# Kernel optimization log

Hardware: AMD Instinct MI355X
Metric: run time of the kernel (lower is better)

Reference implementation:

```python
import jax, jax.numpy as jnp
import numpy as np

D_MODEL = 1024
N_HEADS = 16
D_K = D_MODEL // N_HEADS  # 64
B, T = 2, 2048


def setup_inputs() -> dict:
    key = jax.random.key(0)
    ks = jax.random.split(key, 6)
    s = 0.02
    x = jax.random.normal(ks[0], (B, T, D_MODEL), dtype=jnp.float32)
    # Stacked per-head projection weights, [H, C, d_k] (no bias, mini-gpt style)
    Wq = jax.random.normal(ks[1], (N_HEADS, D_MODEL, D_K), dtype=jnp.float32) * s
    Wk = jax.random.normal(ks[2], (N_HEADS, D_MODEL, D_K), dtype=jnp.float32) * s
    Wv = jax.random.normal(ks[3], (N_HEADS, D_MODEL, D_K), dtype=jnp.float32) * s
    # Output projection, torch nn.Linear(d_model, d_model): y = x @ Wo.T + bo
    Wo = jax.random.normal(ks[4], (D_MODEL, D_MODEL), dtype=jnp.float32) * s
    bo = jax.random.normal(ks[5], (D_MODEL,), dtype=jnp.float32) * s
    return {"x": x, "Wq": Wq, "Wk": Wk, "Wv": Wv, "Wo": Wo, "bo": bo}


def reference(x, Wq, Wk, Wv, Wo, bo):
    Bq, Tq, C = x.shape
    # Batched per-head projections (replaces the per-head Python loop)
    q = jnp.einsum('btc,hck->bhtk', x, Wq)  # [B,H,T,dk]
    k = jnp.einsum('btc,hck->bhtk', x, Wk)
    v = jnp.einsum('btc,hck->bhtk', x, Wv)
    scale = 1.0 / jnp.sqrt(jnp.asarray(D_K, dtype=x.dtype))
    scores = jnp.einsum('bhtk,bhsk->bhts', q, k) * scale  # [B,H,T,T]
    causal = jnp.tril(jnp.ones((Tq, Tq), dtype=bool))
    scores = jnp.where(causal, scores, jnp.asarray(-1e9, dtype=scores.dtype))
    attn = jax.nn.softmax(scores, axis=-1)
    out = jnp.einsum('bhts,bhsk->bhtk', attn, v)  # [B,H,T,dk]
    # concat heads -> [B,T,C]
    out = out.transpose(0, 2, 1, 3).reshape(Bq, Tq, C)
    return jnp.einsum('btc,dc->btd', out, Wo) + bo
```

## Files before the change

kernel.cpp:

```cpp
#include <hip/hip_runtime.h>
#include <hip/hip_bf16.h>


using short8 = __attribute__((ext_vector_type(8))) short;
using f32x4  = __attribute__((ext_vector_type(4))) float;
using fp16x2 = __attribute__((ext_vector_type(2))) __fp16;
using half4  = __attribute__((ext_vector_type(4))) _Float16;
using half8  = __attribute__((ext_vector_type(8))) _Float16;

#define SCALE_LOG2E 0.18033688011112042f

__device__ __forceinline__ unsigned short f2bf(float f) {
    union { float f; unsigned u; } v; v.f = f;
    unsigned r = v.u + 0x7fffu + ((v.u >> 16) & 1u);
    return (unsigned short)(r >> 16);
}

__device__ __forceinline__ void gld16(const unsigned short* gp, unsigned short* lp) {
    __builtin_amdgcn_global_load_lds(
        (const __attribute__((address_space(1))) void*)(gp),
        (__attribute__((address_space(3))) void*)(unsigned int)(unsigned long long)(lp),
        16, 0, 0);
}

__global__ void cvt_bf16(const float* __restrict__ in,
                         unsigned short* __restrict__ out, int n4) {
    int i = blockIdx.x * blockDim.x + threadIdx.x;
    if (i >= n4) return;
    float4 v = ((const float4*)in)[i];
    ushort4 o;
    o.x = f2bf(v.x); o.y = f2bf(v.y); o.z = f2bf(v.z); o.w = f2bf(v.w);
    ((ushort4*)out)[i] = o;
}

__global__ void transpose_w(const float* __restrict__ Wq,
                            const float* __restrict__ Wk,
                            const float* __restrict__ Wv,
                            unsigned short* __restrict__ wfrag) {
    __shared__ float tile[64][65];
    int b = blockIdx.x;
    int cchunk = b & 15;
    int h = (b >> 4) & 15;
    int s = b >> 8;
    const float* W = (s == 0) ? Wq : ((s == 1) ? Wk : Wv);
    float sc = (s == 0) ? SCALE_LOG2E : 1.0f;
    const float* src = W + (h * 1024 + cchunk * 64) * 64;
    int t = threadIdx.x;
    #pragma unroll
    for (int it = 0; it < 4; ++it) {
        int idx = (it * 256 + t) * 4;
        int cc = idx >> 6, kk = idx & 63;
        float4 v = *(const float4*)(src + idx);
        tile[cc][kk + 0] = v.x; tile[cc][kk + 1] = v.y;
        tile[cc][kk + 2] = v.z; tile[cc][kk + 3] = v.w;
    }
    __syncthreads();
    int sh = s * 16 + h;
    #pragma unroll
    for (int p = 0; p < 2; ++p) {
        int slot = p * 256 + t;
        int d   = slot & 63;
        int cc8 = slot >> 6;
        int n16  = sh * 4 + (d >> 4);
        int col  = d & 15;
        int kq   = cchunk * 2 + (cc8 >> 2);
        int quad = cc8 & 3;
        ushort4 lo, hi;
        lo.x = f2bf(tile[cc8 * 8 + 0][d] * sc); lo.y = f2bf(tile[cc8 * 8 + 1][d] * sc);
        lo.z = f2bf(tile[cc8 * 8 + 2][d] * sc); lo.w = f2bf(tile[cc8 * 8 + 3][d] * sc);
        hi.x = f2bf(tile[cc8 * 8 + 4][d] * sc); hi.y = f2bf(tile[cc8 * 8 + 5][d] * sc);
        hi.z = f2bf(tile[cc8 * 8 + 6][d] * sc); hi.w = f2bf(tile[cc8 * 8 + 7][d] * sc);
        unsigned short* dst = wfrag + ((size_t)((n16 * 32 + kq) * 64 + quad * 16 + col)) * 8;
        *(ushort4*)dst = lo;
        *(ushort4*)(dst + 4) = hi;
    }
}

__global__ void wo_frag(const float* __restrict__ Wo,
                        unsigned short* __restrict__ wofrag) {
    int g = blockIdx.x * 256 + threadIdx.x;
    int col  = g & 15;
    int quad = (g >> 4) & 3;
    int kq   = (g >> 6) & 31;
    int n16  = g >> 11;
    const float* src = Wo + (size_t)(n16 * 16 + col) * 1024 + kq * 32 + quad * 8;
    float4 a = *(const float4*)src;
    float4 b = *(const float4*)(src + 4);
    ushort4 lo, hi;
    lo.x = f2bf(a.x); lo.y = f2bf(a.y); lo.z = f2bf(a.z); lo.w = f2bf(a.w);
    hi.x = f2bf(b.x); hi.y = f2bf(b.y); hi.z = f2bf(b.z); hi.w = f2bf(b.w);
    *(ushort4*)(wofrag + (size_t)g * 8)     = lo;
    *(ushort4*)(wofrag + (size_t)g * 8 + 4) = hi;
}

__global__ __launch_bounds__(128, 4) void qkv_gemm(
        const unsigned short* __restrict__ xb,
        const unsigned short* __restrict__ wtf,
        unsigned short* __restrict__ qB,
        unsigned short* __restrict__ kfrag,
        _Float16* __restrict__ vfrag) {
    __shared__ unsigned short Als[64 * 32];
    int wave = threadIdx.x >> 6;
    int lane = threadIdx.x & 63;
    int col  = lane & 15;
    int quad = lane >> 4;
    int ldr = lane >> 2;
    int ldc = ((lane & 3) ^ ((lane >> 3) & 3)) * 8;
    int swq = (quad ^ ((col >> 1) & 3)) * 8;
    int m0 = blockIdx.x * 64;
    int n0 = blockIdx.y * 128 + wave * 64;
    int n16b = n0 >> 4;
    f32x4 acc[4][4] = {};
    for (int k0 = 0; k0 < 1024; k0 += 32) {
        int kq = k0 >> 5;
        __syncthreads();
        short8 bf[4];
        #pragma unroll
        for (int nb = 0; nb < 4; ++nb)
            bf[nb] = *(const short8*)(wtf +
                ((size_t)((n16b + nb) * 32 + kq) * 64 + lane) * 8);
        #pragma unroll
        for (int j = 0; j < 2; ++j) {
            int row = wave * 32 + j * 16;
            gld16(xb + (size_t)(m0 + row + ldr) * 1024 + k0 + ldc, Als + row * 32);
        }
        __syncthreads();
        short8 af[4];
        #pragma unroll
        for (int i = 0; i < 4; ++i)
            af[i] = *(const short8*)(Als + (i * 16 + col) * 32 + swq);
        #pragma unroll
        for (int mb = 0; mb < 4; ++mb)
            #pragma unroll
            for (int nb = 0; nb < 4; ++nb)
                acc[mb][nb] = __builtin_amdgcn_mfma_f32_16x16x32_bf16(
                    af[mb], bf[nb], acc[mb][nb], 0, 0, 0);
    }
    int sel = blockIdx.y >> 3;
    #pragma unroll
    for (int nb = 0; nb < 4; ++nb) {
        int n = n0 + nb * 16 + col;
        int d10 = n & 1023;
        int h_ = d10 >> 6, d = d10 & 63;
        if (sel == 0) {
            #pragma unroll
            for (int mb = 0; mb < 4; ++mb)
                #pragma unroll
                for (int r = 0; r < 4; ++r) {
                    int m = m0 + mb * 16 + quad * 4 + r;
                    int b_ = m >> 11, t_ = m & 2047;
                    qB[((size_t)(b_ * 16 + h_) * 2048 + t_) * 64 + d] =
                        f2bf(acc[mb][nb][r]);
                }
        } else if (sel == 1) {
            int hK = d >> 5, quadk = (d >> 3) & 3, j = d & 7;
            #pragma unroll
            for (int mb = 0; mb < 4; ++mb)
                #pragma unroll
                for (int r = 0; r < 4; ++r) {
                    int m = m0 + mb * 16 + quad * 4 + r;
                    int b_ = m >> 11, t_ = m & 2047;
                    int bh = b_ * 16 + h_;
                    kfrag[((((size_t)bh * 128 + (t_ >> 4)) * 2 + hK) * 64 +
                           quadk * 16 + (t_ & 15)) * 8 + j] = f2bf(acc[mb][nb][r]);
                }
        } else {
            int nbv = d >> 4, colv = d & 15;
            #pragma unroll
            for (int mb = 0; mb < 4; ++mb) {
                int m = m0 + mb * 16 + quad * 4;
                int b_ = m >> 11, t_ = m & 2047;
                int bh = b_ * 16 + h_;
                half4 hv;
                hv[0] = (_Float16)acc[mb][nb][0]; hv[1] = (_Float16)acc[mb][nb][1];
                hv[2] = (_Float16)acc[mb][nb][2]; hv[3] = (_Float16)acc[mb][nb][3];
                *(half4*)(vfrag + ((((size_t)bh * 64 + (t_ >> 5)) * 4 + nbv) * 64 +
                          ((t_ >> 2) & 3) * 16 + colv) * 8 + ((t_ >> 4) & 1) * 4) = hv;
            }
        }
    }
}

__global__ __launch_bounds__(128, 4) void oproj(
        const unsigned short* __restrict__ A,
        const unsigned short* __restrict__ wof,
        const float* __restrict__ bo,
        float* __restrict__ y) {
    __shared__ unsigned short Als[32 * 32];
    int wave = threadIdx.x >> 6;
    int lane = threadIdx.x & 63;
    int col  = lane & 15;
    int quad = lane >> 4;
    int ldr = lane >> 2;
    int ldc = ((lane & 3) ^ ((lane >> 3) & 3)) * 8;
    int swq = (quad ^ ((col >> 1) & 3)) * 8;
    int m0 = blockIdx.x * 32;
    int n0 = blockIdx.y * 128 + wave * 64;
    int n16b = n0 >> 4;
    f32x4 acc[2][4] = {};
    for (int k0 = 0; k0 < 1024; k0 += 32) {
        int kq = k0 >> 5;
        __syncthreads();
        short8 bf[4];
        #pragma unroll
        for (int nb = 0; nb < 4; ++nb)
            bf[nb] = *(const short8*)(wof +
                ((size_t)((n16b + nb) * 32 + kq) * 64 + lane) * 8);
        gld16(A + (size_t)(m0 + wave * 16 + ldr) * 1024 + k0 + ldc,
              Als + (wave * 16) * 32);
        __syncthreads();
        short8 af[2];
        #pragma unroll
        for (int i = 0; i < 2; ++i)
            af[i] = *(const short8*)(Als + (i * 16 + col) * 32 + swq);
        #pragma unroll
        for (int mb = 0; mb < 2; ++mb)
            #pragma unroll
            for (int nb = 0; nb < 4; ++nb)
                acc[mb][nb] = __builtin_amdgcn_mfma_f32_16x16x32_bf16(
                    af[mb], bf[nb], acc[mb][nb], 0, 0, 0);
    }
    #pragma unroll
    for (int nb = 0; nb < 4; ++nb) {
        int n = n0 + nb * 16 + col;
        float bias = bo[n];
        #pragma unroll
        for (int mb = 0; mb < 2; ++mb)
            #pragma unroll
            for (int r = 0; r < 4; ++r) {
                int m = m0 + mb * 16 + quad * 4 + r;
                y[(size_t)m * 1024 + n] = acc[mb][nb][r] + bias;
            }
    }
}

__global__ __launch_bounds__(256, 3) void attn(
        const unsigned short* __restrict__ qB,
        const unsigned short* __restrict__ kfrag,
        const _Float16* __restrict__ vfrag,
        unsigned short* __restrict__ aout) {
    __shared__ float O_comb[2][64][33];
    __shared__ float L_comb[2][2][2][16];
    int wave = threadIdx.x >> 6;
    int lane = threadIdx.x & 63;
    int col  = lane & 15;
    int quad = lane >> 4;
    int sl     = wave >> 1;
    int parity = wave & 1;
    int bh   = blockIdx.x & 31;
    int pairidx = 31 - (blockIdx.x >> 5);
    int strip = pairidx * 2 + sl;
    int q0 = strip * 32;
    const unsigned short* q = qB + (size_t)bh * 2048 * 64;
    const unsigned short* kf_base = kfrag + (size_t)bh * 128 * 2 * 512;
    const _Float16*       vf_base = vfrag + (size_t)bh * 64 * 4 * 512;

    short8 qf[2][2];
    #pragma unroll
    for (int qb = 0; qb < 2; ++qb)
        #pragma unroll
        for (int h = 0; h < 2; ++h)
            qf[qb][h] = *(const short8*)(q + (size_t)(q0 + qb * 16 + col) * 64 + h * 32 + quad * 8);

    f32x4 o[2][4] = {};
    float l[2] = {0.f, 0.f};

    struct KV { short8 kf[2][2]; half8 vv[4]; };
    KV bufA, bufB;

    auto load_half = [&](int it, int kv32, KV& b) {
        int K16 = it * 4 + kv32 * 2;
        #pragma unroll
        for (int p = 0; p < 2; ++p)
            #pragma unroll
            for (int h = 0; h < 2; ++h)
                b.kf[p][h] = *(const short8*)(kf_base +
                    (((size_t)(K16 + p) * 2 + h) * 64 + lane) * 8);
        #pragma unroll
        for (int nb = 0; nb < 4; ++nb)
            b.vv[nb] = *(const half8*)(vf_base +
                (((size_t)(it * 2 + kv32) * 4 + nb) * 64 + lane) * 8);
    };

    auto compute_half = [&](int it, int kv32, KV& b) {
        int kv0 = it * 64;
        bool diag = (kv0 + 63 > q0);
        #pragma unroll
        for (int par = 0; par < 2; ++par) {
            int kvbase = kv0 + kv32 * 32 + par * 16;
            f32x4 st[2] = {};
            #pragma unroll
            for (int qb = 0; qb < 2; ++qb) {
                st[qb] = __builtin_amdgcn_mfma_f32_16x16x32_bf16(b.kf[par][0], qf[qb][0], st[qb], 0, 0, 0);
                st[qb] = __builtin_amdgcn_mfma_f32_16x16x32_bf16(b.kf[par][1], qf[qb][1], st[qb], 0, 0, 0);
            }
            #pragma unroll
            for (int qb = 0; qb < 2; ++qb) {
                float p0 = __builtin_amdgcn_exp2f(st[qb][0]);
                float p1 = __builtin_amdgcn_exp2f(st[qb][1]);
                float p2 = __builtin_amdgcn_exp2f(st[qb][2]);
                float p3 = __builtin_amdgcn_exp2f(st[qb][3]);
                if (diag) {
                    int qg  = q0 + qb * 16 + col;
                    int kvg = kvbase + quad * 4;
                    p0 = (kvg + 0 > qg) ? 0.f : p0;
                    p1 = (kvg + 1 > qg) ? 0.f : p1;
                    p2 = (kvg + 2 > qg) ? 0.f : p2;
                    p3 = (kvg + 3 > qg) ? 0.f : p3;
                }
                l[qb] += (p0 + p1) + (p2 + p3);
                union { fp16x2 h2[2]; half4 h4; } cvt;
                cvt.h2[0] = __builtin_amdgcn_cvt_pkrtz(p0, p1);
                cvt.h2[1] = __builtin_amdgcn_cvt_pkrtz(p2, p3);
                half4 pf = cvt.h4;
                #pragma unroll
                for (int nb = 0; nb < 4; ++nb) {
                    half4 vf = (par == 0)
                        ? __builtin_shufflevector(b.vv[nb], b.vv[nb], 0, 1, 2, 3)
                        : __builtin_shufflevector(b.vv[nb], b.vv[nb], 4, 5, 6, 7);
                    o[qb][nb] = __builtin_amdgcn_mfma_f32_16x16x16f16(pf, vf, o[qb][nb], 0, 0, 0);
                }
            }
        }
    };

    int n_iter = (q0 + 95) >> 6;
    if (parity < n_iter) load_half(parity, 0, bufA);
    for (int it = parity; it < n_iter; it += 2) {
        load_half(it, 1, bufB);
        compute_half(it, 0, bufA);
        if (it + 2 < n_iter) load_half(it + 2, 0, bufA);
        compute_half(it, 1, bufB);
    }

    #pragma unroll
    for (int qb = 0; qb < 2; ++qb) {
        float lr = l[qb];
        lr += __shfl_xor(lr, 16);
        lr += __shfl_xor(lr, 32);
        l[qb] = lr;
    }
    if (quad == 0) {
        L_comb[sl][parity][0][col] = l[0];
        L_comb[sl][parity][1][col] = l[1];
    }
    if (parity == 1) {
        #pragma unroll
        for (int qb = 0; qb < 2; ++qb)
            #pragma unroll
            for (int nb = 0; nb < 4; ++nb)
                #pragma unroll
                for (int r = 0; r < 4; ++r)
                    O_comb[sl][lane][qb * 16 + nb * 4 + r] = o[qb][nb][r];
    }
    __syncthreads();
    if (parity == 0) {
        int b_ = bh >> 4, h_ = bh & 15;
        #pragma unroll
        for (int qb = 0; qb < 2; ++qb)
            #pragma unroll
            for (int r = 0; r < 4; ++r) {
                int qi = quad * 4 + r;
                float inv_l = 1.0f / (L_comb[sl][0][qb][qi] + L_comb[sl][1][qb][qi]);
                int t_ = q0 + qb * 16 + qi;
                #pragma unroll
                for (int nb = 0; nb < 4; ++nb) {
                    float ov = o[qb][nb][r] + O_comb[sl][lane][qb * 16 + nb * 4 + r];
                    aout[(size_t)(b_ * 2048 + t_) * 1024 + h_ * 64 + nb * 16 + col] =
                        f2bf(ov * inv_l);
                }
            }
    }
}

extern "C" void kernel_launch(void* const* d_in, const int* in_sizes, int n_in,
                              void* d_out, int out_size, void* d_ws, size_t ws_size,
                              hipStream_t stream) {
    const float* x  = (const float*)d_in[0];
    const float* Wq = (const float*)d_in[1];
    const float* Wk = (const float*)d_in[2];
    const float* Wv = (const float*)d_in[3];
    const float* Wo = (const float*)d_in[4];
    const float* bo = (const float*)d_in[5];
    float* y = (float*)d_out;

    unsigned short* xb    = (unsigned short*)d_ws;
    unsigned short* Wtf   = xb    + 4194304;
    unsigned short* Wof   = Wtf   + 3145728;
    unsigned short* qBb   = Wof   + 1048576;
    unsigned short* kfr   = qBb   + 4194304;
    unsigned short* vfr   = kfr   + 4194304;
    unsigned short* aout  = vfr   + 4194304;

    cvt_bf16<<<4096, 256, 0, stream>>>(x, xb, 1048576);
    transpose_w<<<768, 256, 0, stream>>>(Wq, Wk, Wv, Wtf);
    wo_frag<<<512, 256, 0, stream>>>(Wo, Wof);
    qkv_gemm<<<dim3(64, 24), 128, 0, stream>>>(xb, Wtf, qBb, kfr, (_Float16*)vfr);
    attn<<<1024, 256, 0, stream>>>(qBb, kfr, (const _Float16*)vfr, aout);
    oproj<<<dim3(128, 8), 128, 0, stream>>>(aout, Wof, bo, y);
}
```

Measured before the change: 169.5 us.

## Merge prep kernels and double-buffer QKV and output projection GEMMs

Folds the three preprocessing kernels (x cast, QKV weight fragment transpose, Wo fragment build) into one launch that dispatches on block index, which cuts launch overhead. Both projection GEMMs switch to double-buffered LDS staging with register-prefetched B fragments, so the loads for the next K step overlap the MFMA work on the current one. The QKV GEMM also moves to 256-thread blocks covering 128 rows, so each B fragment feeds more rows, at the cost of twice the LDS and fewer blocks.

```diff
diff --git a/kernel.cpp b/kernel.cpp
--- a/kernel.cpp
+++ b/kernel.cpp
@@ -23,83 +23,85 @@
         16, 0, 0);
 }
 
-__global__ void cvt_bf16(const float* __restrict__ in,
-                         unsigned short* __restrict__ out, int n4) {
-    int i = blockIdx.x * blockDim.x + threadIdx.x;
-    if (i >= n4) return;
-    float4 v = ((const float4*)in)[i];
-    ushort4 o;
-    o.x = f2bf(v.x); o.y = f2bf(v.y); o.z = f2bf(v.z); o.w = f2bf(v.w);
-    ((ushort4*)out)[i] = o;
-}
-
-__global__ void transpose_w(const float* __restrict__ Wq,
-                            const float* __restrict__ Wk,
-                            const float* __restrict__ Wv,
-                            unsigned short* __restrict__ wfrag) {
+__global__ void prep(const float* __restrict__ x,
+                     const float* __restrict__ Wq,
+                     const float* __restrict__ Wk,
+                     const float* __restrict__ Wv,
+                     const float* __restrict__ Wo,
+                     unsigned short* __restrict__ xb,
+                     unsigned short* __restrict__ wfrag,
+                     unsigned short* __restrict__ wofrag) {
     __shared__ float tile[64][65];
-    int b = blockIdx.x;
-    int cchunk = b & 15;
-    int h = (b >> 4) & 15;
-    int s = b >> 8;
-    const float* W = (s == 0) ? Wq : ((s == 1) ? Wk : Wv);
-    float sc = (s == 0) ? SCALE_LOG2E : 1.0f;
-    const float* src = W + (h * 1024 + cchunk * 64) * 64;
+    int blk = blockIdx.x;
     int t = threadIdx.x;
-    #pragma unroll
-    for (int it = 0; it < 4; ++it) {
-        int idx = (it * 256 + t) * 4;
-        int cc = idx >> 6, kk = idx & 63;
-        float4 v = *(const float4*)(src + idx);
-        tile[cc][kk + 0] = v.x; tile[cc][kk + 1] = v.y;
-        tile[cc][kk + 2] = v.z; tile[cc][kk + 3] = v.w;
-    }
-    __syncthreads();
-    int sh = s * 16 + h;
-    #pragma unroll
-    for (int p = 0; p < 2; ++p) {
-        int slot = p * 256 + t;
-        int d   = slot & 63;
-        int cc8 = slot >> 6;
-        int n16  = sh * 4 + (d >> 4);
-        int col  = d & 15;
-        int kq   = cchunk * 2 + (cc8 >> 2);
-        int quad = cc8 & 3;
+    if (blk < 768) {
+        int b = blk;
+        int cchunk = b & 15;
+        int h = (b >> 4) & 15;
+        int s = b >> 8;
+        const float* W = (s == 0) ? Wq : ((s == 1) ? Wk : Wv);
+        float sc = (s == 0) ? SCALE_LOG2E : 1.0f;
+        const float* src = W + (h * 1024 + cchunk * 64) * 64;
+        #pragma unroll
+        for (int it = 0; it < 4; ++it) {
+            int idx = (it * 256 + t) * 4;
+            int cc = idx >> 6, kk = idx & 63;
+            float4 v = *(const float4*)(src + idx);
+            tile[cc][kk + 0] = v.x; tile[cc][kk + 1] = v.y;
+            tile[cc][kk + 2] = v.z; tile[cc][kk + 3] = v.w;
+        }
+        __syncthreads();
+        int sh = s * 16 + h;
+        #pragma unroll
+        for (int p = 0; p < 2; ++p) {
+            int slot = p * 256 + t;
+            int d   = slot & 63;
+            int cc8 = slot >> 6;
+            int n16  = sh * 4 + (d >> 4);
+            int col  = d & 15;
+            int kq   = cchunk * 2 + (cc8 >> 2);
+            int quad = cc8 & 3;
+            ushort4 lo, hi;
+            lo.x = f2bf(tile[cc8 * 8 + 0][d] * sc); lo.y = f2bf(tile[cc8 * 8 + 1][d] * sc);
+            lo.z = f2bf(tile[cc8 * 8 + 2][d] * sc); lo.w = f2bf(tile[cc8 * 8 + 3][d] * sc);
+            hi.x = f2bf(tile[cc8 * 8 + 4][d] * sc); hi.y = f2bf(tile[cc8 * 8 + 5][d] * sc);
+            hi.z = f2bf(tile[cc8 * 8 + 6][d] * sc); hi.w = f2bf(tile[cc8 * 8 + 7][d] * sc);
+            unsigned short* dst = wfrag + ((size_t)((n16 * 32 + kq) * 64 + quad * 16 + col)) * 8;
+            *(ushort4*)dst = lo;
+            *(ushort4*)(dst + 4) = hi;
+        }
+    } else if (blk < 1280) {
+        int g = (blk - 768) * 256 + t;
+        int col  = g & 15;
+        int quad = (g >> 4) & 3;
+        int kq   = (g >> 6) & 31;
+        int n16  = g >> 11;
+        const float* src = Wo + (size_t)(n16 * 16 + col) * 1024 + kq * 32 + quad * 8;
+        float4 a = *(const float4*)src;
+        float4 b2 = *(const float4*)(src + 4);
         ushort4 lo, hi;
-        lo.x = f2bf(tile[cc8 * 8 + 0][d] * sc); lo.y = f2bf(tile[cc8 * 8 + 1][d] * sc);
-        lo.z = f2bf(tile[cc8 * 8 + 2][d] * sc); lo.w = f2bf(tile[cc8 * 8 + 3][d] * sc);
-        hi.x = f2bf(tile[cc8 * 8 + 4][d] * sc); hi.y = f2bf(tile[cc8 * 8 + 5][d] * sc);
-        hi.z = f2bf(tile[cc8 * 8 + 6][d] * sc); hi.w = f2bf(tile[cc8 * 8 + 7][d] * sc);
-        unsigned short* dst = wfrag + ((size_t)((n16 * 32 + kq) * 64 + quad * 16 + col)) * 8;
-        *(ushort4*)dst = lo;
-        *(ushort4*)(dst + 4) = hi;
-    }
-}
-
-__global__ void wo_frag(const float* __restrict__ Wo,
-                        unsigned short* __restrict__ wofrag) {
-    int g = blockIdx.x * 256 + threadIdx.x;
-    int col  = g & 15;
-    int quad = (g >> 4) & 3;
-    int kq   = (g >> 6) & 31;
-    int n16  = g >> 11;
-    const float* src = Wo + (size_t)(n16 * 16 + col) * 1024 + kq * 32 + quad * 8;
-    float4 a = *(const float4*)src;
-    float4 b = *(const float4*)(src + 4);
-    ushort4 lo, hi;
-    lo.x = f2bf(a.x); lo.y = f2bf(a.y); lo.z = f2bf(a.z); lo.w = f2bf(a.w);
-    hi.x = f2bf(b.x); hi.y = f2bf(b.y); hi.z = f2bf(b.z); hi.w = f2bf(b.w);
-    *(ushort4*)(wofrag + (size_t)g * 8)     = lo;
-    *(ushort4*)(wofrag + (size_t)g * 8 + 4) = hi;
-}
-
-__global__ __launch_bounds__(128, 4) void qkv_gemm(
+        lo.x = f2bf(a.x); lo.y = f2bf(a.y); lo.z = f2bf(a.z); lo.w = f2bf(a.w);
+        hi.x = f2bf(b2.x); hi.y = f2bf(b2.y); hi.z = f2bf(b2.z); hi.w = f2bf(b2.w);
+        *(ushort4*)(wofrag + (size_t)g * 8)     = lo;
+        *(ushort4*)(wofrag + (size_t)g * 8 + 4) = hi;
+    } else {
+        int i = (blk - 1280) * 256 + t;
+        if (i < 1048576) {
+            float4 v = ((const float4*)x)[i];
+            ushort4 o;
+            o.x = f2bf(v.x); o.y = f2bf(v.y); o.z = f2bf(v.z); o.w = f2bf(v.w);
+            ((ushort4*)xb)[i] = o;
+        }
+    }
+}
+
+__global__ __launch_bounds__(256, 3) void qkv_gemm(
         const unsigned short* __restrict__ xb,
         const unsigned short* __restrict__ wtf,
         unsigned short* __restrict__ qB,
         unsigned short* __restrict__ kfrag,
         _Float16* __restrict__ vfrag) {
-    __shared__ unsigned short Als[64 * 32];
+    __shared__ unsigned short Als[2][128 * 32];
     int wave = threadIdx.x >> 6;
     int lane = threadIdx.x & 63;
     int col  = lane & 15;
@@ -107,35 +109,55 @@
     int ldr = lane >> 2;
     int ldc = ((lane & 3) ^ ((lane >> 3) & 3)) * 8;
     int swq = (quad ^ ((col >> 1) & 3)) * 8;
-    int m0 = blockIdx.x * 64;
-    int n0 = blockIdx.y * 128 + wave * 64;
+    int mq = wave >> 1;
+    int nq = wave & 1;
+    int m0 = blockIdx.x * 128;
+    int n0 = blockIdx.y * 128 + nq * 64;
     int n16b = n0 >> 4;
     f32x4 acc[4][4] = {};
-    for (int k0 = 0; k0 < 1024; k0 += 32) {
-        int kq = k0 >> 5;
-        __syncthreads();
-        short8 bf[4];
+
+    auto stageA = [&](int buf, int k0) {
+        #pragma unroll
+        for (int j = 0; j < 2; ++j) {
+            int row = wave * 32 + j * 16;
+            gld16(xb + (size_t)(m0 + row + ldr) * 1024 + k0 + ldc,
+                  &Als[buf][row * 32]);
+        }
+    };
+    auto loadB = [&](int kq, short8 (&bf)[4]) {
         #pragma unroll
         for (int nb = 0; nb < 4; ++nb)
             bf[nb] = *(const short8*)(wtf +
                 ((size_t)((n16b + nb) * 32 + kq) * 64 + lane) * 8);
-        #pragma unroll
-        for (int j = 0; j < 2; ++j) {
-            int row = wave * 32 + j * 16;
-            gld16(xb + (size_t)(m0 + row + ldr) * 1024 + k0 + ldc, Als + row * 32);
-        }
-        __syncthreads();
+    };
+    auto compute = [&](const unsigned short* ls, short8 (&bf)[4]) {
         short8 af[4];
         #pragma unroll
         for (int i = 0; i < 4; ++i)
-            af[i] = *(const short8*)(Als + (i * 16 + col) * 32 + swq);
+            af[i] = *(const short8*)(ls + (mq * 64 + i * 16 + col) * 32 + swq);
         #pragma unroll
         for (int mb = 0; mb < 4; ++mb)
             #pragma unroll
             for (int nb = 0; nb < 4; ++nb)
                 acc[mb][nb] = __builtin_amdgcn_mfma_f32_16x16x32_bf16(
                     af[mb], bf[nb], acc[mb][nb], 0, 0, 0);
-    }
+    };
+
+    short8 bfA[4], bfB[4];
+    stageA(0, 0);
+    loadB(0, bfA);
+    __syncthreads();
+    for (int kq = 0; kq < 32; kq += 2) {
+        stageA(1, (kq + 1) << 5);
+        loadB(kq + 1, bfB);
+        compute(Als[0], bfA);
+        __syncthreads();
+        if (kq + 2 < 32) { stageA(0, (kq + 2) << 5); loadB(kq + 2, bfA); }
+        compute(Als[1], bfB);
+        __syncthreads();
+    }
+
+    int wm0 = m0 + mq * 64;
     int sel = blockIdx.y >> 3;
     #pragma unroll
     for (int nb = 0; nb < 4; ++nb) {
@@ -147,7 +169,7 @@
             for (int mb = 0; mb < 4; ++mb)
                 #pragma unroll
                 for (int r = 0; r < 4; ++r) {
-                    int m = m0 + mb * 16 + quad * 4 + r;
+                    int m = wm0 + mb * 16 + quad * 4 + r;
                     int b_ = m >> 11, t_ = m & 2047;
                     qB[((size_t)(b_ * 16 + h_) * 2048 + t_) * 64 + d] =
                         f2bf(acc[mb][nb][r]);
@@ -158,7 +180,7 @@
             for (int mb = 0; mb < 4; ++mb)
                 #pragma unroll
                 for (int r = 0; r < 4; ++r) {
-                    int m = m0 + mb * 16 + quad * 4 + r;
+                    int m = wm0 + mb * 16 + quad * 4 + r;
                     int b_ = m >> 11, t_ = m & 2047;
                     int bh = b_ * 16 + h_;
                     kfrag[((((size_t)bh * 128 + (t_ >> 4)) * 2 + hK) * 64 +
@@ -168,7 +190,7 @@
             int nbv = d >> 4, colv = d & 15;
             #pragma unroll
             for (int mb = 0; mb < 4; ++mb) {
-                int m = m0 + mb * 16 + quad * 4;
+                int m = wm0 + mb * 16 + quad * 4;
                 int b_ = m >> 11, t_ = m & 2047;
                 int bh = b_ * 16 + h_;
                 half4 hv;
@@ -186,7 +208,7 @@
         const unsigned short* __restrict__ wof,
         const float* __restrict__ bo,
         float* __restrict__ y) {
-    __shared__ unsigned short Als[32 * 32];
+    __shared__ unsigned short Als[2][32 * 32];
     int wave = threadIdx.x >> 6;
     int lane = threadIdx.x & 63;
     int col  = lane & 15;
@@ -198,28 +220,44 @@
     int n0 = blockIdx.y * 128 + wave * 64;
     int n16b = n0 >> 4;
     f32x4 acc[2][4] = {};
-    for (int k0 = 0; k0 < 1024; k0 += 32) {
-        int kq = k0 >> 5;
-        __syncthreads();
-        short8 bf[4];
+
+    auto stageA = [&](int buf, int k0) {
+        gld16(A + (size_t)(m0 + wave * 16 + ldr) * 1024 + k0 + ldc,
+              &Als[buf][wave * 16 * 32]);
+    };
+    auto loadB = [&](int kq, short8 (&bf)[4]) {
         #pragma unroll
         for (int nb = 0; nb < 4; ++nb)
             bf[nb] = *(const short8*)(wof +
                 ((size_t)((n16b + nb) * 32 + kq) * 64 + lane) * 8);
-        gld16(A + (size_t)(m0 + wave * 16 + ldr) * 1024 + k0 + ldc,
-              Als + (wave * 16) * 32);
-        __syncthreads();
+    };
+    auto compute = [&](const unsigned short* ls, short8 (&bf)[4]) {
         short8 af[2];
         #pragma unroll
         for (int i = 0; i < 2; ++i)
-            af[i] = *(const short8*)(Als + (i * 16 + col) * 32 + swq);
+            af[i] = *(const short8*)(ls + (i * 16 + col) * 32 + swq);
         #pragma unroll
         for (int mb = 0; mb < 2; ++mb)
             #pragma unroll
             for (int nb = 0; nb < 4; ++nb)
                 acc[mb][nb] = __builtin_amdgcn_mfma_f32_16x16x32_bf16(
                     af[mb], bf[nb], acc[mb][nb], 0, 0, 0);
-    }
+    };
+
+    short8 bfA[4], bfB[4];
+    stageA(0, 0);
+    loadB(0, bfA);
+    __syncthreads();
+    for (int kq = 0; kq < 32; kq += 2) {
+        stageA(1, (kq + 1) << 5);
+        loadB(kq + 1, bfB);
+        compute(Als[0], bfA);
+        __syncthreads();
+        if (kq + 2 < 32) { stageA(0, (kq + 2) << 5); loadB(kq + 2, bfA); }
+        compute(Als[1], bfB);
+        __syncthreads();
+    }
+
     #pragma unroll
     for (int nb = 0; nb < 4; ++nb) {
         int n = n0 + nb * 16 + col;
@@ -392,10 +430,8 @@
     unsigned short* vfr   = kfr   + 4194304;
     unsigned short* aout  = vfr   + 4194304;
 
-    cvt_bf16<<<4096, 256, 0, stream>>>(x, xb, 1048576);
-    transpose_w<<<768, 256, 0, stream>>>(Wq, Wk, Wv, Wtf);
-    wo_frag<<<512, 256, 0, stream>>>(Wo, Wof);
-    qkv_gemm<<<dim3(64, 24), 128, 0, stream>>>(xb, Wtf, qBb, kfr, (_Float16*)vfr);
+    prep<<<5376, 256, 0, stream>>>(x, Wq, Wk, Wv, Wo, xb, Wtf, Wof);
+    qkv_gemm<<<dim3(32, 24), 256, 0, stream>>>(xb, Wtf, qBb, kfr, (_Float16*)vfr);
     attn<<<1024, 256, 0, stream>>>(qBb, kfr, (const _Float16*)vfr, aout);
     oproj<<<dim3(128, 8), 128, 0, stream>>>(aout, Wof, bo, y);
 }
```

Measured after the change: 180.0 us. +6.2%, slower.
